# Performance work log

Hardware: AMD Instinct MI355X
Metric: run time of the kernel (lower is better)

The kernel has to match this reference:

```python
import jax, jax.numpy as jnp
import numpy as np

N = 50000      # nodes
E = 800000     # edges
R = 8          # relations
DIN, DH, DOUT = 128, 128, 64
EPS = 1e-5     # BatchNorm eps


def setup_inputs() -> dict:
    key = jax.random.key(0)
    ks = jax.random.split(key, 24)
    w = lambda k, shape, fan_in: jax.random.normal(k, shape, jnp.float32) / np.sqrt(fan_in)
    x = jax.random.normal(ks[0], (N, DIN), jnp.float32)
    edge_index = jax.random.randint(ks[1], (2, E), 0, N, dtype=jnp.int64)
    edge_type = jax.random.randint(ks[2], (E,), 0, R, dtype=jnp.int64)
    return {
        "x": x, "edge_index": edge_index, "edge_type": edge_type,
        # layer 1: RGCN(DIN->DH) + BN
        "W1": w(ks[3], (R, DIN, DH), DIN), "Wr1": w(ks[4], (DIN, DH), DIN), "b1": jnp.zeros((DH,), jnp.float32),
        "g1": jnp.ones((DH,), jnp.float32), "be1": jnp.zeros((DH,), jnp.float32),
        "rm1": 0.1 * jax.random.normal(ks[5], (DH,), jnp.float32),
        "rv1": jax.random.uniform(ks[6], (DH,), jnp.float32, 0.5, 1.5),
        # layer 2: RGCN(DH->DH) + BN
        "W2": w(ks[7], (R, DH, DH), DH), "Wr2": w(ks[8], (DH, DH), DH), "b2": jnp.zeros((DH,), jnp.float32),
        "g2": jnp.ones((DH,), jnp.float32), "be2": jnp.zeros((DH,), jnp.float32),
        "rm2": 0.1 * jax.random.normal(ks[9], (DH,), jnp.float32),
        "rv2": jax.random.uniform(ks[10], (DH,), jnp.float32, 0.5, 1.5),
        # layer 3: RGCN(DH->DOUT)
        "W3": w(ks[11], (R, DH, DOUT), DH), "Wr3": w(ks[12], (DH, DOUT), DH), "b3": jnp.zeros((DOUT,), jnp.float32),
    }


def rgcn_layer(x, W, Wroot, b, src, dst, et):
    # PyG RGCNConv: per-relation linear transform, per-relation MEAN aggregation
    # over incoming edges, plus root transform and bias.
    nR, nN, H = W.shape[0], x.shape[0], W.shape[2]
    h = jnp.einsum('nd,rdh->rnh', x, W)          # [R,N,H] per-relation transform
    msg = h[et, src]                             # [E,H] gather per edge
    seg = dst * nR + et                          # segment key = (node, relation)
    sums = jax.ops.segment_sum(msg, seg, num_segments=nN * nR)
    cnt = jax.ops.segment_sum(jnp.ones((seg.shape[0],), x.dtype), seg, num_segments=nN * nR)
    mean = sums / jnp.maximum(cnt, 1.0)[:, None]
    agg = mean.reshape(nN, nR, H).sum(axis=1)    # sum over relations
    return agg + x @ Wroot + b


def batchnorm(x, g, b, rm, rv):
    # eval-mode BatchNorm1d with running stats
    return (x - rm) * jax.lax.rsqrt(rv + EPS) * g + b


def reference(x, edge_index, edge_type,
              W1, Wr1, b1, g1, be1, rm1, rv1,
              W2, Wr2, b2, g2, be2, rm2, rv2,
              W3, Wr3, b3):
    src, dst = edge_index[0], edge_index[1]
    h = rgcn_layer(x, W1, Wr1, b1, src, dst, edge_type)
    h = jax.nn.relu(batchnorm(h, g1, be1, rm1, rv1))  # dropout: eval mode = identity
    h = rgcn_layer(h, W2, Wr2, b2, src, dst, edge_type)
    h = jax.nn.relu(batchnorm(h, g2, be2, rm2, rv2))
    h = rgcn_layer(h, W3, Wr3, b3, src, dst, edge_type)
    return jax.nn.sigmoid(h)
```

## Files before the change

### kernel.cpp

```cpp
#include <hip/hip_runtime.h>

typedef _Float16 f16;
typedef __attribute__((ext_vector_type(8))) _Float16 half8;
typedef __attribute__((ext_vector_type(2))) _Float16 half2v;
typedef __attribute__((ext_vector_type(4))) float float4v;

#define NNODES 50000
#define NEDGES 800000
#define NREL 8
#define NRSEG (NNODES * NREL)
#define KDIM 1152
#define CAP 16
#define CAPQ (CAP / 4)
#define NT64 ((NNODES + 63) / 64)

__global__ void bucket_fill(const int* __restrict__ src, const int* __restrict__ dst,
                            const int* __restrict__ et, int* __restrict__ cnt,
                            int* __restrict__ esrc) {
    int e = blockIdx.x * blockDim.x + threadIdx.x;
    if (e < NEDGES) {
        int s = dst[e] * NREL + et[e];
        int p = atomicAdd(&cnt[s], 1);
        if (p < CAP) esrc[s * CAP + p] = src[e];
    }
}

__global__ void setup_misc(const float* __restrict__ x, f16* __restrict__ x16,
                           const float* __restrict__ W1, const float* __restrict__ Wr1,
                           const float* __restrict__ W2, const float* __restrict__ Wr2,
                           const float* __restrict__ W3, const float* __restrict__ Wr3,
                           f16* __restrict__ Bt, int* __restrict__ cnt) {
    int t = blockIdx.x * blockDim.x + threadIdx.x;
    if (t < NNODES * 64) {
        float2 v = ((const float2*)x)[t];
        half2v o = {(f16)v.x, (f16)v.y};
        ((half2v*)x16)[t] = o;
        return;
    }
    int idx = t - NNODES * 64;
    if (idx < 320 * KDIM) {
        int hg = idx / KDIM, k = idx - hg * KDIM;
        const float *W, *Wr;
        int h, H;
        if (hg < 128)      { W = W1; Wr = Wr1; h = hg;       H = 128; }
        else if (hg < 256) { W = W2; Wr = Wr2; h = hg - 128; H = 128; }
        else               { W = W3; Wr = Wr3; h = hg - 256; H = 64;  }
        float v = (k < 1024) ? W[(size_t)k * H + h] : Wr[(size_t)(k - 1024) * H + h];
        Bt[idx] = (f16)v;
        return;
    }
    int z = idx - 320 * KDIM;
    if (z < NRSEG / 4) ((int4*)cnt)[z] = (int4){0, 0, 0, 0};
}

template <int H, int MODE>
__global__ __launch_bounds__(256, 4) void fused_layer(
    const f16* __restrict__ act, const f16* __restrict__ Bt,
    const int* __restrict__ cnt, const int* __restrict__ esrc,
    const float* __restrict__ bias, const float* __restrict__ g,
    const float* __restrict__ be, const float* __restrict__ rm,
    const float* __restrict__ rv, f16* __restrict__ hout, float* __restrict__ fout) {
    constexpr int NT = H / 16;
    __shared__ f16 Ws[H][128];
    const int tid = threadIdx.x;
    const int wave = tid >> 6, lane = tid & 63;
    const int l15 = lane & 15, quad = lane >> 4;
    const int m0 = blockIdx.x * 64 + wave * 16;
    int node = m0 + l15;
    node = node < NNODES ? node : NNODES - 1;

    int4 cq0 = ((const int4*)cnt)[node * 2];
    int4 cq1 = ((const int4*)cnt)[node * 2 + 1];
    int cnts[8] = {cq0.x, cq0.y, cq0.z, cq0.w, cq1.x, cq1.y, cq1.z, cq1.w};
    const int4* bq_base = (const int4*)esrc + (size_t)node * NREL * CAPQ;

    float4v acc[NT];
#pragma unroll
    for (int j = 0; j < NT; ++j) acc[j] = (float4v){0.f, 0.f, 0.f, 0.f};

    int4 qp0 = bq_base[0];
    int4 qp1 = bq_base[CAPQ];
    half8 af_root[4];

#pragma unroll
    for (int r = 0; r < 9; ++r) {
        __syncthreads();
#pragma unroll
        for (int i = 0; i < NT; ++i) {
            int G = i * 256 + tid;
            int row = G >> 4, gg = G & 15;
            half8 v = *(const half8*)(Bt + (size_t)row * KDIM + r * 128 + gg * 8);
            *(half8*)&Ws[row][((gg ^ (row & 7))) * 8] = v;
        }
        float c[32];
        if (r < 8) {
            int truelen = cnts[r];
            int len = truelen < CAP ? truelen : CAP;
            float inv = truelen > 1 ? 1.f / (float)truelen : 1.f;
            const int4* bq = bq_base + r * CAPQ;
            int4 q0 = qp0;
            qp0 = qp1;
            if (r < 6) qp1 = bq_base[(r + 2) * CAPQ];
#pragma unroll
            for (int t = 0; t < 32; ++t) c[t] = 0.f;
            for (int j4 = 0; j4 < (len + 3) >> 2; ++j4) {
                int4 q = (j4 == 0) ? q0 : bq[j4];
                int ids[4] = {q.x, q.y, q.z, q.w};
                int base = j4 * 4;
#pragma unroll
                for (int t = 0; t < 4; ++t) {
                    if (base + t < len) {
                        const half8* rp = (const half8*)(act + (size_t)ids[t] * 128 + quad * 8);
                        half8 v0 = rp[0], v1 = rp[4], v2 = rp[8], v3 = rp[12];
#pragma unroll
                        for (int u = 0; u < 8; ++u) {
                            c[u] += (float)v0[u];
                            c[8 + u] += (float)v1[u];
                            c[16 + u] += (float)v2[u];
                            c[24 + u] += (float)v3[u];
                        }
                    }
                }
            }
#pragma unroll
            for (int t = 0; t < 32; ++t) c[t] *= inv;
        } else {
#pragma unroll
            for (int ks = 0; ks < 4; ++ks)
                af_root[ks] = *(const half8*)(act + (size_t)node * 128 + ks * 32 + quad * 8);
        }
        __syncthreads();
#pragma unroll
        for (int ks = 0; ks < 4; ++ks) {
            half8 af;
            if (r < 8) {
#pragma unroll
                for (int u = 0; u < 8; ++u) af[u] = (f16)c[ks * 8 + u];
            } else {
                af = af_root[ks];
            }
#pragma unroll
            for (int nt = 0; nt < NT; ++nt) {
                int row = nt * 16 + l15;
                half8 bf = *(const half8*)&Ws[row][(((ks * 4 + quad) ^ (row & 7))) * 8];
                acc[nt] = __builtin_amdgcn_mfma_f32_16x16x32_f16(af, bf, acc[nt], 0, 0, 0);
            }
        }
    }

#pragma unroll
    for (int nt = 0; nt < NT; ++nt) {
        int col = nt * 16 + l15;
        float alpha, beta;
        if (MODE == 0) {
            float sc = g[col] * rsqrtf(rv[col] + 1e-5f);
            alpha = sc;
            beta = (bias[col] - rm[col]) * sc + be[col];
        } else {
            alpha = 1.f;
            beta = bias[col];
        }
#pragma unroll
        for (int rg = 0; rg < 4; ++rg) {
            int row = m0 + quad * 4 + rg;
            if (row < NNODES) {
                float v = fmaf(acc[nt][rg], alpha, beta);
                if (MODE == 0) {
                    hout[(size_t)row * H + col] = (f16)fmaxf(v, 0.f);
                } else {
                    fout[(size_t)row * H + col] = 1.f / (1.f + __expf(-v));
                }
            }
        }
    }
}

extern "C" void kernel_launch(void* const* d_in, const int* in_sizes, int n_in,
                              void* d_out, int out_size, void* d_ws, size_t ws_size,
                              hipStream_t stream) {
    (void)in_sizes; (void)n_in; (void)out_size; (void)ws_size;
    const float* x   = (const float*)d_in[0];
    const int* ei    = (const int*)d_in[1];
    const int* et    = (const int*)d_in[2];
    const float* W1  = (const float*)d_in[3];
    const float* Wr1 = (const float*)d_in[4];
    const float* b1  = (const float*)d_in[5];
    const float* g1  = (const float*)d_in[6];
    const float* be1 = (const float*)d_in[7];
    const float* rm1 = (const float*)d_in[8];
    const float* rv1 = (const float*)d_in[9];
    const float* W2  = (const float*)d_in[10];
    const float* Wr2 = (const float*)d_in[11];
    const float* b2  = (const float*)d_in[12];
    const float* g2  = (const float*)d_in[13];
    const float* be2 = (const float*)d_in[14];
    const float* rm2 = (const float*)d_in[15];
    const float* rv2 = (const float*)d_in[16];
    const float* W3  = (const float*)d_in[17];
    const float* Wr3 = (const float*)d_in[18];
    const float* b3  = (const float*)d_in[19];
    const int* src = ei;
    const int* dst = ei + NEDGES;
    float* out = (float*)d_out;

    char* ws = (char*)d_ws;
    size_t off = 0;
    auto alloc = [&](size_t bytes) -> void* {
        off = (off + 255) & ~(size_t)255;
        void* p = ws + off;
        off += bytes;
        return p;
    };
    int* cnt  = (int*)alloc((size_t)NRSEG * 4);
    int* esrc = (int*)alloc((size_t)NRSEG * CAP * 4);
    f16* x16  = (f16*)alloc((size_t)NNODES * 128 * 2);
    f16* ha   = (f16*)alloc((size_t)NNODES * 128 * 2);
    f16* hb   = (f16*)alloc((size_t)NNODES * 128 * 2);
    f16* Bt   = (f16*)alloc((size_t)320 * KDIM * 2);

    const int SETUP_T = NNODES * 64 + 320 * KDIM + NRSEG / 4;
    setup_misc<<<(SETUP_T + 255) / 256, 256, 0, stream>>>(
        x, x16, W1, Wr1, W2, Wr2, W3, Wr3, Bt, cnt);
    bucket_fill<<<(NEDGES + 255) / 256, 256, 0, stream>>>(src, dst, et, cnt, esrc);

    fused_layer<128, 0><<<NT64, 256, 0, stream>>>(x16, Bt, cnt, esrc,
                                                  b1, g1, be1, rm1, rv1, ha, nullptr);
    fused_layer<128, 0><<<NT64, 256, 0, stream>>>(ha, Bt + (size_t)128 * KDIM, cnt, esrc,
                                                  b2, g2, be2, rm2, rv2, hb, nullptr);
    fused_layer<64, 1><<<NT64, 256, 0, stream>>>(hb, Bt + (size_t)256 * KDIM, cnt, esrc,
                                                 b3, nullptr, nullptr, nullptr, nullptr,
                                                 nullptr, out);
}
```

Baseline: 417.0 us.

## Software-pipeline neighbor row gathers across relations and relax launch bounds

Restructures the per-relation gather so the first three neighbor rows of the next relation are loaded while the current relation is being accumulated, and the root row is loaded during the last relation. The goal is to hide gather latency behind arithmetic and the shared-memory weight staging. This needs more registers, so launch bounds drop from 4 to 3 blocks per CU, which lowers occupancy. Fallback loads of the node's own row are issued for empty slots, adding some wasted traffic.

Result: slower. 548.2 us (+31.5%).

```diff
diff --git a/kernel.cpp b/kernel.cpp
--- a/kernel.cpp
+++ b/kernel.cpp
@@ -54,7 +54,7 @@
 }
 
 template <int H, int MODE>
-__global__ __launch_bounds__(256, 4) void fused_layer(
+__global__ __launch_bounds__(256, 3) void fused_layer(
     const f16* __restrict__ act, const f16* __restrict__ Bt,
     const int* __restrict__ cnt, const int* __restrict__ esrc,
     const float* __restrict__ bias, const float* __restrict__ g,
@@ -78,8 +78,20 @@
 #pragma unroll
     for (int j = 0; j < NT; ++j) acc[j] = (float4v){0.f, 0.f, 0.f, 0.f};
 
-    int4 qp0 = bq_base[0];
-    int4 qp1 = bq_base[CAPQ];
+    auto issue = [&](half8* v, int id) {
+        const half8* rp = (const half8*)(act + (size_t)id * 128 + quad * 8);
+        v[0] = rp[0]; v[1] = rp[4]; v[2] = rp[8]; v[3] = rp[12];
+    };
+
+    int4 qh0 = bq_base[0];
+    int4 qh1 = bq_base[CAPQ];
+    half8 e0[4], e1[4], e2[4];
+    {
+        int len = cnts[0] < CAP ? cnts[0] : CAP;
+        issue(e0, len > 0 ? qh0.x : node);
+        issue(e1, len > 1 ? qh0.y : node);
+        issue(e2, len > 2 ? qh0.z : node);
+    }
     half8 af_root[4];
 
 #pragma unroll
@@ -97,37 +109,60 @@
             int truelen = cnts[r];
             int len = truelen < CAP ? truelen : CAP;
             float inv = truelen > 1 ? 1.f / (float)truelen : 1.f;
+            int4 qh = qh0;
+
+            half8 e3[4];
+            issue(e3, len > 3 ? qh.w : node);
+
+            auto accum = [&](const half8* v) {
+#pragma unroll
+                for (int u = 0; u < 8; ++u) {
+                    c[u] += (float)v[0][u];
+                    c[8 + u] += (float)v[1][u];
+                    c[16 + u] += (float)v[2][u];
+                    c[24 + u] += (float)v[3][u];
+                }
+            };
+
+#pragma unroll
+            for (int t = 0; t < 32; ++t) c[t] = 0.f;
+            if (len > 0) accum(e0);
+            if (len > 1) accum(e1);
+            if (len > 2) accum(e2);
+
+            qh0 = qh1;
+            if (r < 6) qh1 = bq_base[(r + 2) * CAPQ];
+            if (r < 7) {
+                int nl = cnts[r + 1];
+                nl = nl < CAP ? nl : CAP;
+                issue(e0, nl > 0 ? qh0.x : node);
+                issue(e1, nl > 1 ? qh0.y : node);
+                issue(e2, nl > 2 ? qh0.z : node);
+            } else {
+#pragma unroll
+                for (int ks = 0; ks < 4; ++ks)
+                    af_root[ks] = *(const half8*)(act + (size_t)node * 128 + ks * 32 + quad * 8);
+            }
+
+            if (len > 3) accum(e3);
+
             const int4* bq = bq_base + r * CAPQ;
-            int4 q0 = qp0;
-            qp0 = qp1;
-            if (r < 6) qp1 = bq_base[(r + 2) * CAPQ];
-#pragma unroll
-            for (int t = 0; t < 32; ++t) c[t] = 0.f;
-            for (int j4 = 0; j4 < (len + 3) >> 2; ++j4) {
-                int4 q = (j4 == 0) ? q0 : bq[j4];
+            int nj = (len + 3) >> 2;
+            for (int j4 = 1; j4 < nj; ++j4) {
+                int4 q = bq[j4];
                 int ids[4] = {q.x, q.y, q.z, q.w};
                 int base = j4 * 4;
 #pragma unroll
                 for (int t = 0; t < 4; ++t) {
                     if (base + t < len) {
-                        const half8* rp = (const half8*)(act + (size_t)ids[t] * 128 + quad * 8);
-                        half8 v0 = rp[0], v1 = rp[4], v2 = rp[8], v3 = rp[12];
-#pragma unroll
-                        for (int u = 0; u < 8; ++u) {
-                            c[u] += (float)v0[u];
-                            c[8 + u] += (float)v1[u];
-                            c[16 + u] += (float)v2[u];
-                            c[24 + u] += (float)v3[u];
-                        }
+                        half8 v[4];
+                        issue(v, ids[t]);
+                        accum(v);
                     }
                 }
             }
 #pragma unroll
             for (int t = 0; t < 32; ++t) c[t] *= inv;
-        } else {
-#pragma unroll
-            for (int ks = 0; ks < 4; ++ks)
-                af_root[ks] = *(const half8*)(act + (size_t)node * 128 + ks * 32 + quad * 8);
         }
         __syncthreads();
 #pragma unroll
```
